# Optimization experiments

Hardware: AMD Instinct MI355X
Metric: run time of the kernel (lower is better)

Reference implementation:

```python
import jax, jax.numpy as jnp
import numpy as np

B, CIN, H, W = 32, 512, 64, 64
HID, A, C = 256, 9, 20
M = 65536


def setup_inputs() -> dict:
    key = jax.random.key(0)
    k = jax.random.split(key, 7)
    N = B * A * H * W
    features = jax.random.normal(k[0], (B, CIN, H, W), jnp.float32)
    W1 = jax.random.normal(k[1], (HID, CIN), jnp.float32) * 0.02
    b1 = jnp.zeros((HID,), jnp.float32)
    W2 = jax.random.normal(k[2], (5 * A + C, HID), jnp.float32) * 0.02
    b2 = jnp.zeros((5 * A + C,), jnp.float32)
    pos_anchor_idx = jax.random.randint(k[3], (M,), 0, N, jnp.int64 if jax.config.read('jax_enable_x64') else jnp.int32)
    neg_anchor_idx = jax.random.randint(k[4], (M,), 0, N, jnp.int64 if jax.config.read('jax_enable_x64') else jnp.int32)
    return {"features": features, "W1": W1, "b1": b1, "W2": W2, "b2": b2,
            "pos_anchor_idx": pos_anchor_idx, "neg_anchor_idx": neg_anchor_idx}


def reference(features, W1, b1, W2, b2, pos_anchor_idx, neg_anchor_idx):
    Bb, Cin, Hh, Ww = features.shape
    # 1x1 convs are channel GEMMs
    h = jnp.einsum('bchw,oc->bohw', features, W1) + b1[None, :, None, None]
    h = jax.nn.leaky_relu(h, 0.01)  # Dropout2d identity at inference
    out = jnp.einsum('bchw,oc->bohw', h, W2) + b2[None, :, None, None]
    class_scores = out[:, 5 * A:, :, :]                      # (B, C, H, W)
    anchor = out[:, :5 * A, :, :].reshape(Bb, A, 5, Hh, Ww)   # (B, A, 5, H, W)
    conf = jax.nn.sigmoid(anchor[:, :, 0:1])                  # (B, A, 1, H, W)
    off = anchor[:, :, 1:]                                    # (B, A, 4, H, W)
    off = jnp.concatenate([jax.nn.sigmoid(off[:, :, :2]) - 0.5, off[:, :, 2:]], axis=2)
    # extraction: flat layout is b*A*H*W + a*H*W + h*W + w (permute 0,1,3,4,2)
    off_flat = off.transpose(0, 1, 3, 4, 2).reshape(-1, 4)
    conf_flat = conf.transpose(0, 1, 3, 4, 2).reshape(-1, 1)
    offsets = off_flat[pos_anchor_idx]                        # (M, 4)
    conf_out = jnp.concatenate([conf_flat[pos_anchor_idx], conf_flat[neg_anchor_idx]], axis=0)  # (2M, 1)
    # class scores: expand over A is a pure broadcast, so index by (b, spatial) directly
    b_idx = pos_anchor_idx // (A * Hh * Ww)
    sp = pos_anchor_idx % (Hh * Ww)
    cls_flat = class_scores.transpose(0, 2, 3, 1).reshape(Bb * Hh * Ww, -1)
    class_out = cls_flat[b_idx * (Hh * Ww) + sp]              # (M, C)
    return conf_out, offsets, class_out
```

## Files before the change

### kernel.cpp

```cpp
#include <hip/hip_runtime.h>
#include <hip/hip_bf16.h>

typedef __attribute__((ext_vector_type(8)))  __bf16 bf16x8;
typedef __attribute__((ext_vector_type(4)))  __bf16 bf16x4;
typedef __attribute__((ext_vector_type(16))) float  f32x16;
typedef __attribute__((ext_vector_type(4)))  float  f32x4;

#define B_    32
#define CIN   512
#define HID   256
#define HW    4096
#define NA    9
#define NCH   65
#define NPADC 96
#define BN    128
#define M_    65536
#define NTOT  (B_*NA*HW)

#define BAR() do {                                          \
    asm volatile("s_waitcnt lgkmcnt(0)" ::: "memory");      \
    __builtin_amdgcn_s_barrier();                           \
    __builtin_amdgcn_sched_barrier(0);                      \
} while (0)


static __device__ __forceinline__ float sigf(float v) {
    return 1.f / (1.f + __expf(-v));
}

__global__ void prep_weights(const float* __restrict__ W1, const float* __restrict__ W2,
                             unsigned short* __restrict__ W1bt, unsigned short* __restrict__ W2p) {
    int i = blockIdx.x * 256 + threadIdx.x;
    if (i < 16*256*32) {
        int kt = i >> 13, o = (i >> 5) & 255, kk = i & 31;
        __bf16 h = (__bf16)W1[o*CIN + kt*32 + kk];
        W1bt[i] = __builtin_bit_cast(unsigned short, h);
    } else {
        int j = i - 16*256*32;
        if (j < NPADC*HID) {
            int o = j >> 8, c = j & 255;
            float v = (o < NCH) ? W2[o*HID + c] : 0.f;
            __bf16 h = (__bf16)v;
            W2p[j] = __builtin_bit_cast(unsigned short, h);
        }
    }
}

__launch_bounds__(256, 2)
__global__ void fused_mlp(const float* __restrict__ feat,
                          const float* __restrict__ b1,
                          const float* __restrict__ b2,
                          const unsigned short* __restrict__ W1bt,
                          const unsigned short* __restrict__ W2p,
                          float* __restrict__ conf_d,
                          unsigned short* __restrict__ off_w,
                          unsigned short* __restrict__ cls_w) {
    __shared__ __align__(16) unsigned char smem[65536];

    const int tid  = threadIdx.x;
    const int w    = tid >> 6;
    const int lane = tid & 63;
    const int lr   = lane & 31;
    const int lh   = lane >> 5;
    const int bidx = blockIdx.x >> 5;
    const int hw0  = (blockIdx.x & 31) * BN;

    const float* fb = feat + (size_t)bidx * CIN * HW + hw0;

    const int sB  = tid & 127;
    const int kgB = tid >> 7;

    f32x16 acc[2][4];
#pragma unroll
    for (int m = 0; m < 2; ++m)
#pragma unroll
        for (int n = 0; n < 4; ++n) acc[m][n] = (f32x16)0.f;

    float  pb[2][16];
    bf16x8 aw[2][4];

    auto issueB = [&](int kt, int s) {
#pragma unroll
        for (int q = 0; q < 2; ++q) {
            const float* src = fb + (size_t)(kt*32 + (kgB + 2*q)*8) * HW + sB;
#pragma unroll
            for (int j = 0; j < 8; ++j) pb[s][q*8 + j] = src[(size_t)j * HW];
        }
    };
    auto issueA = [&](int kt, int s) {
#pragma unroll
        for (int kk = 0; kk < 2; ++kk)
#pragma unroll
            for (int m = 0; m < 2; ++m)
                aw[s][kk*2 + m] = *(const bf16x8*)(W1bt + kt*8192 + (64*w + 32*m + lr)*32 + kk*16 + lh*8);
    };
    auto storeB = [&](int s) {
        unsigned short* Bst = (unsigned short*)(smem + s*10240);
#pragma unroll
        for (int q = 0; q < 2; ++q) {
            bf16x8 v8;
#pragma unroll
            for (int j = 0; j < 8; ++j) v8[j] = (__bf16)pb[s][q*8 + j];
            *(bf16x8*)(Bst + sB*40 + (kgB + 2*q)*8) = v8;
        }
    };

    issueA(0, 0); issueB(0, 0); issueB(1, 1);
    storeB(0);
    BAR();

#pragma unroll
    for (int kt = 0; kt < 16; ++kt) {
        const int cur = kt & 1, nxt = cur ^ 1;
        if (kt + 1 < 16) issueA(kt + 1, nxt);
        if (kt + 2 < 16) issueB(kt + 2, cur);
        const unsigned short* Bst = (const unsigned short*)(smem + cur*10240);
#pragma unroll
        for (int kk = 0; kk < 2; ++kk) {
            bf16x8 a0 = aw[cur][kk*2 + 0];
            bf16x8 a1 = aw[cur][kk*2 + 1];
#pragma unroll
            for (int n = 0; n < 4; ++n) {
                bf16x8 bv = *(const bf16x8*)(Bst + (32*n + lr)*40 + kk*16 + lh*8);
                acc[0][n] = __builtin_amdgcn_mfma_f32_32x32x16_bf16(a0, bv, acc[0][n], 0, 0, 0);
                acc[1][n] = __builtin_amdgcn_mfma_f32_32x32x16_bf16(a1, bv, acc[1][n], 0, 0, 0);
            }
        }
        if (kt + 1 < 16) storeB(nxt);
        BAR();
    }

#pragma unroll
    for (int m = 0; m < 2; ++m)
#pragma unroll
        for (int n = 0; n < 4; ++n) {
            int col = 32*n + lr;
            unsigned cswz = (unsigned)((col & 7) << 4);
#pragma unroll
            for (int g = 0; g < 4; ++g) {
                int rbase = 64*w + 32*m + 8*g + 4*lh;
                f32x4 b1v = *(const f32x4*)(b1 + rbase);
                bf16x4 pk;
#pragma unroll
                for (int r = 0; r < 4; ++r) {
                    float v = acc[m][n][4*g + r] + b1v[r];
                    v = v > 0.f ? v : 0.01f * v;
                    pk[r] = (__bf16)v;
                }
                unsigned addr = (unsigned)(col*512 + rbase*2) ^ cswz;
                *(bf16x4*)(smem + addr) = pk;
            }
        }
    BAR();

    f32x16 acc2[3];
#pragma unroll
    for (int m = 0; m < 3; ++m) acc2[m] = (f32x16)0.f;
    const int col2 = 32*w + lr;
    const unsigned cswz2 = (unsigned)((col2 & 7) << 4);
    for (int kt2 = 0; kt2 < 8; ++kt2) {
#pragma unroll
        for (int kk = 0; kk < 2; ++kk) {
            int k0 = kt2*32 + kk*16 + lh*8;
            bf16x8 bv = *(const bf16x8*)(smem + ((unsigned)(col2*512 + k0*2) ^ cswz2));
#pragma unroll
            for (int m = 0; m < 3; ++m) {
                bf16x8 av = *(const bf16x8*)(W2p + (32*m + lr)*256 + k0);
                acc2[m] = __builtin_amdgcn_mfma_f32_32x32x16_bf16(av, bv, acc2[m], 0, 0, 0);
            }
        }
    }

    BAR();
    float* so = (float*)smem;
#pragma unroll
    for (int m = 0; m < 3; ++m)
#pragma unroll
        for (int g = 0; g < 4; ++g) {
            int rbase = 32*m + 8*g + 4*lh;
            if (rbase <= 64) {
#pragma unroll
                for (int r = 0; r < 4; ++r) {
                    int row = rbase + r;
                    if (row < NCH) so[row*128 + col2] = acc2[m][4*g + r] + b2[row];
                }
            }
        }
    BAR();

    {
        const int p   = tid & 127;
        const int phw = hw0 + p;
        const int b9  = bidx * NA;
        if (tid < 128) {
#pragma unroll
            for (int a = 0; a < 9; ++a) {
                float v0 = so[(5*a+0)*128 + p];
                float v1 = so[(5*a+1)*128 + p];
                float v2 = so[(5*a+2)*128 + p];
                float v3 = so[(5*a+3)*128 + p];
                float v4 = so[(5*a+4)*128 + p];
                int abase = ((b9 + a) << 12) + phw;
                conf_d[abase] = sigf(v0);
                bf16x4 o;
                o[0] = (__bf16)(sigf(v1) - 0.5f);
                o[1] = (__bf16)(sigf(v2) - 0.5f);
                o[2] = (__bf16)v3;
                o[3] = (__bf16)v4;
                *(bf16x4*)(off_w + ((size_t)abase << 2)) = o;
            }
        } else {
            unsigned short* dst = cls_w + ((size_t)((bidx << 12) + phw) << 5);
#pragma unroll
            for (int q = 0; q < 4; ++q) {
                bf16x8 v;
#pragma unroll
                for (int r = 0; r < 8; ++r) {
                    int c = q*8 + r;
                    v[r] = (c < 20) ? (__bf16)so[(45 + c)*128 + p] : (__bf16)0.f;
                }
                *(bf16x8*)(dst + q*8) = v;
            }
        }
    }
}

__global__ void gather_all(const int* __restrict__ pos, const int* __restrict__ neg,
                           const float* __restrict__ conf_d,
                           const unsigned short* __restrict__ off_w,
                           const unsigned short* __restrict__ cls_w,
                           float* __restrict__ out) {
    int t = blockIdx.x * 256 + threadIdx.x;
    if (t < 2*M_) {
        int idx = (t < M_) ? pos[t] : neg[t - M_];
        out[t] = conf_d[idx];
    } else if (t < 3*M_) {
        int i = t - 2*M_;
        int p = pos[i];
        bf16x4 o = *(const bf16x4*)(off_w + ((size_t)p << 2));
        f32x4 f;
        f[0] = (float)o[0]; f[1] = (float)o[1];
        f[2] = (float)o[2]; f[3] = (float)o[3];
        *(f32x4*)(out + 2*(size_t)M_ + 4*(size_t)i) = f;
    } else {
        int i = t - 3*M_;
        int p = pos[i];
        int hw = p & 4095;
        int b  = (p >> 12) / 9;
        const unsigned short* src = cls_w + ((size_t)((b << 12) + hw) << 5);
        float* dst = out + 6*(size_t)M_ + 20*(size_t)i;
        bf16x8 v0 = *(const bf16x8*)(src);
        bf16x8 v1 = *(const bf16x8*)(src + 8);
        bf16x4 v2 = *(const bf16x4*)(src + 16);
        f32x4 f;
        f[0] = (float)v0[0]; f[1] = (float)v0[1]; f[2] = (float)v0[2]; f[3] = (float)v0[3];
        *(f32x4*)(dst) = f;
        f[0] = (float)v0[4]; f[1] = (float)v0[5]; f[2] = (float)v0[6]; f[3] = (float)v0[7];
        *(f32x4*)(dst + 4) = f;
        f[0] = (float)v1[0]; f[1] = (float)v1[1]; f[2] = (float)v1[2]; f[3] = (float)v1[3];
        *(f32x4*)(dst + 8) = f;
        f[0] = (float)v1[4]; f[1] = (float)v1[5]; f[2] = (float)v1[6]; f[3] = (float)v1[7];
        *(f32x4*)(dst + 12) = f;
        f[0] = (float)v2[0]; f[1] = (float)v2[1]; f[2] = (float)v2[2]; f[3] = (float)v2[3];
        *(f32x4*)(dst + 16) = f;
    }
}

extern "C" void kernel_launch(void* const* d_in, const int* in_sizes, int n_in,
                              void* d_out, int out_size, void* d_ws, size_t ws_size,
                              hipStream_t stream) {
    const float* feat = (const float*)d_in[0];
    const float* W1   = (const float*)d_in[1];
    const float* b1   = (const float*)d_in[2];
    const float* W2   = (const float*)d_in[3];
    const float* b2   = (const float*)d_in[4];
    const int*   pos  = (const int*)d_in[5];
    const int*   neg  = (const int*)d_in[6];
    float* out = (float*)d_out;

    char* ws = (char*)d_ws;
    unsigned short* W1bt = (unsigned short*)ws;
    unsigned short* W2p  = (unsigned short*)(ws + 262144);
    float*          conf_d = (float*)(ws + 311296);
    unsigned short* off_w  = (unsigned short*)(ws + 5029888);
    unsigned short* cls_w  = (unsigned short*)(ws + 14467072);

    prep_weights<<<608, 256, 0, stream>>>(W1, W2, W1bt, W2p);
    fused_mlp<<<1024, 256, 0, stream>>>(feat, b1, b2, W1bt, W2p, conf_d, off_w, cls_w);
    gather_all<<<1024, 256, 0, stream>>>(pos, neg, conf_d, off_w, cls_w, out);
}
```

Measured before the change: 92.18 us.

## Double block tile to 256 pixels with 512 threads and split second GEMM per half

The fused MLP kernel now uses 512-thread blocks, each covering 256 spatial positions, and arranges its 8 waves as 4 hidden-row groups by 2 pixel halves. Each W1 fragment loaded from global memory is reused across twice as many pixels, and the grid drops from 1024 to 512 blocks. The second GEMM and the epilogue run twice, once per 128-pixel half, with all 8 waves sharing each half (W2 padded to 128 rows). This adds extra barriers and serialises the two halves. Fewer, larger blocks also risk lower occupancy and worse tail balance on the CUs.

```diff
diff --git a/kernel.cpp b/kernel.cpp
--- a/kernel.cpp
+++ b/kernel.cpp
@@ -12,8 +12,8 @@
 #define HW    4096
 #define NA    9
 #define NCH   65
-#define NPADC 96
-#define BN    128
+#define NPADC 128
+#define BN    256
 #define M_    65536
 #define NTOT  (B_*NA*HW)
 
@@ -46,7 +46,7 @@
     }
 }
 
-__launch_bounds__(256, 2)
+__launch_bounds__(512, 2)
 __global__ void fused_mlp(const float* __restrict__ feat,
                           const float* __restrict__ b1,
                           const float* __restrict__ b2,
@@ -62,13 +62,15 @@
     const int lane = tid & 63;
     const int lr   = lane & 31;
     const int lh   = lane >> 5;
-    const int bidx = blockIdx.x >> 5;
-    const int hw0  = (blockIdx.x & 31) * BN;
+    const int mg   = w >> 1;
+    const int ng   = w & 1;
+    const int bidx = blockIdx.x >> 4;
+    const int hw0  = (blockIdx.x & 15) * BN;
 
     const float* fb = feat + (size_t)bidx * CIN * HW + hw0;
 
-    const int sB  = tid & 127;
-    const int kgB = tid >> 7;
+    const int sB  = tid & 255;
+    const int kgB = tid >> 8;
 
     f32x16 acc[2][4];
 #pragma unroll
@@ -92,10 +94,10 @@
         for (int kk = 0; kk < 2; ++kk)
 #pragma unroll
             for (int m = 0; m < 2; ++m)
-                aw[s][kk*2 + m] = *(const bf16x8*)(W1bt + kt*8192 + (64*w + 32*m + lr)*32 + kk*16 + lh*8);
+                aw[s][kk*2 + m] = *(const bf16x8*)(W1bt + kt*8192 + (64*mg + 32*m + lr)*32 + kk*16 + lh*8);
     };
     auto storeB = [&](int s) {
-        unsigned short* Bst = (unsigned short*)(smem + s*10240);
+        unsigned short* Bst = (unsigned short*)(smem + s*20480);
 #pragma unroll
         for (int q = 0; q < 2; ++q) {
             bf16x8 v8;
@@ -114,14 +116,14 @@
         const int cur = kt & 1, nxt = cur ^ 1;
         if (kt + 1 < 16) issueA(kt + 1, nxt);
         if (kt + 2 < 16) issueB(kt + 2, cur);
-        const unsigned short* Bst = (const unsigned short*)(smem + cur*10240);
+        const unsigned short* Bst = (const unsigned short*)(smem + cur*20480);
 #pragma unroll
         for (int kk = 0; kk < 2; ++kk) {
             bf16x8 a0 = aw[cur][kk*2 + 0];
             bf16x8 a1 = aw[cur][kk*2 + 1];
 #pragma unroll
             for (int n = 0; n < 4; ++n) {
-                bf16x8 bv = *(const bf16x8*)(Bst + (32*n + lr)*40 + kk*16 + lh*8);
+                bf16x8 bv = *(const bf16x8*)(Bst + (128*ng + 32*n + lr)*40 + kk*16 + lh*8);
                 acc[0][n] = __builtin_amdgcn_mfma_f32_32x32x16_bf16(a0, bv, acc[0][n], 0, 0, 0);
                 acc[1][n] = __builtin_amdgcn_mfma_f32_32x32x16_bf16(a1, bv, acc[1][n], 0, 0, 0);
             }
@@ -131,97 +133,104 @@
     }
 
 #pragma unroll
-    for (int m = 0; m < 2; ++m)
-#pragma unroll
-        for (int n = 0; n < 4; ++n) {
-            int col = 32*n + lr;
-            unsigned cswz = (unsigned)((col & 7) << 4);
+    for (int p = 0; p < 2; ++p) {
+        if (ng == p) {
+#pragma unroll
+            for (int m = 0; m < 2; ++m)
+#pragma unroll
+                for (int n = 0; n < 4; ++n) {
+                    int c = 32*n + lr;
+                    unsigned cswz = (unsigned)((c & 7) << 4);
+#pragma unroll
+                    for (int g = 0; g < 4; ++g) {
+                        int rbase = 64*mg + 32*m + 8*g + 4*lh;
+                        f32x4 b1v = *(const f32x4*)(b1 + rbase);
+                        bf16x4 pk;
+#pragma unroll
+                        for (int r = 0; r < 4; ++r) {
+                            float v = acc[m][n][4*g + r] + b1v[r];
+                            v = v > 0.f ? v : 0.01f * v;
+                            pk[r] = (__bf16)v;
+                        }
+                        *(bf16x4*)(smem + ((unsigned)(c*512 + rbase*2) ^ cswz)) = pk;
+                    }
+                }
+        }
+        BAR();
+
+        f32x16 acc2[2];
+#pragma unroll
+        for (int m = 0; m < 2; ++m) acc2[m] = (f32x16)0.f;
+        const int colh = w & 3, rowh = w >> 2;
+        const int col2 = 32*colh + lr;
+        const unsigned cswz2 = (unsigned)((col2 & 7) << 4);
+#pragma unroll
+        for (int kt2 = 0; kt2 < 8; ++kt2) {
+#pragma unroll
+            for (int kk = 0; kk < 2; ++kk) {
+                int k0 = kt2*32 + kk*16 + lh*8;
+                bf16x8 bv2 = *(const bf16x8*)(smem + ((unsigned)(col2*512 + k0*2) ^ cswz2));
+#pragma unroll
+                for (int m = 0; m < 2; ++m) {
+                    bf16x8 av = *(const bf16x8*)(W2p + (64*rowh + 32*m + lr)*256 + k0);
+                    acc2[m] = __builtin_amdgcn_mfma_f32_32x32x16_bf16(av, bv2, acc2[m], 0, 0, 0);
+                }
+            }
+        }
+        BAR();
+
+        float* so = (float*)smem;
+#pragma unroll
+        for (int m = 0; m < 2; ++m)
 #pragma unroll
             for (int g = 0; g < 4; ++g) {
-                int rbase = 64*w + 32*m + 8*g + 4*lh;
-                f32x4 b1v = *(const f32x4*)(b1 + rbase);
-                bf16x4 pk;
-#pragma unroll
-                for (int r = 0; r < 4; ++r) {
-                    float v = acc[m][n][4*g + r] + b1v[r];
-                    v = v > 0.f ? v : 0.01f * v;
-                    pk[r] = (__bf16)v;
-                }
-                unsigned addr = (unsigned)(col*512 + rbase*2) ^ cswz;
-                *(bf16x4*)(smem + addr) = pk;
+                int rbase = 64*rowh + 32*m + 8*g + 4*lh;
+                if (rbase <= 64) {
+#pragma unroll
+                    for (int r = 0; r < 4; ++r) {
+                        int row = rbase + r;
+                        if (row < NCH) so[row*128 + col2] = acc2[m][4*g + r] + b2[row];
+                    }
+                }
             }
-        }
-    BAR();
-
-    f32x16 acc2[3];
-#pragma unroll
-    for (int m = 0; m < 3; ++m) acc2[m] = (f32x16)0.f;
-    const int col2 = 32*w + lr;
-    const unsigned cswz2 = (unsigned)((col2 & 7) << 4);
-    for (int kt2 = 0; kt2 < 8; ++kt2) {
-#pragma unroll
-        for (int kk = 0; kk < 2; ++kk) {
-            int k0 = kt2*32 + kk*16 + lh*8;
-            bf16x8 bv = *(const bf16x8*)(smem + ((unsigned)(col2*512 + k0*2) ^ cswz2));
-#pragma unroll
-            for (int m = 0; m < 3; ++m) {
-                bf16x8 av = *(const bf16x8*)(W2p + (32*m + lr)*256 + k0);
-                acc2[m] = __builtin_amdgcn_mfma_f32_32x32x16_bf16(av, bv, acc2[m], 0, 0, 0);
+        BAR();
+
+        {
+            const int pp  = tid & 127;
+            const int phw = hw0 + 128*p + pp;
+            const int b9  = bidx * NA;
+            if (tid < 128) {
+#pragma unroll
+                for (int a = 0; a < 9; ++a) {
+                    float v0 = so[(5*a+0)*128 + pp];
+                    float v1 = so[(5*a+1)*128 + pp];
+                    float v2 = so[(5*a+2)*128 + pp];
+                    float v3 = so[(5*a+3)*128 + pp];
+                    float v4 = so[(5*a+4)*128 + pp];
+                    int abase = ((b9 + a) << 12) + phw;
+                    conf_d[abase] = sigf(v0);
+                    bf16x4 o;
+                    o[0] = (__bf16)(sigf(v1) - 0.5f);
+                    o[1] = (__bf16)(sigf(v2) - 0.5f);
+                    o[2] = (__bf16)v3;
+                    o[3] = (__bf16)v4;
+                    *(bf16x4*)(off_w + ((size_t)abase << 2)) = o;
+                }
+            } else if (tid < 256) {
+                unsigned short* dst = cls_w + ((size_t)((bidx << 12) + phw) << 5);
+#pragma unroll
+                for (int q = 0; q < 4; ++q) {
+                    bf16x8 v;
+#pragma unroll
+                    for (int r = 0; r < 8; ++r) {
+                        int c = q*8 + r;
+                        v[r] = (c < 20) ? (__bf16)so[(45 + c)*128 + pp] : (__bf16)0.f;
+                    }
+                    *(bf16x8*)(dst + q*8) = v;
+                }
             }
         }
-    }
-
-    BAR();
-    float* so = (float*)smem;
-#pragma unroll
-    for (int m = 0; m < 3; ++m)
-#pragma unroll
-        for (int g = 0; g < 4; ++g) {
-            int rbase = 32*m + 8*g + 4*lh;
-            if (rbase <= 64) {
-#pragma unroll
-                for (int r = 0; r < 4; ++r) {
-                    int row = rbase + r;
-                    if (row < NCH) so[row*128 + col2] = acc2[m][4*g + r] + b2[row];
-                }
-            }
-        }
-    BAR();
-
-    {
-        const int p   = tid & 127;
-        const int phw = hw0 + p;
-        const int b9  = bidx * NA;
-        if (tid < 128) {
-#pragma unroll
-            for (int a = 0; a < 9; ++a) {
-                float v0 = so[(5*a+0)*128 + p];
-                float v1 = so[(5*a+1)*128 + p];
-                float v2 = so[(5*a+2)*128 + p];
-                float v3 = so[(5*a+3)*128 + p];
-                float v4 = so[(5*a+4)*128 + p];
-                int abase = ((b9 + a) << 12) + phw;
-                conf_d[abase] = sigf(v0);
-                bf16x4 o;
-                o[0] = (__bf16)(sigf(v1) - 0.5f);
-                o[1] = (__bf16)(sigf(v2) - 0.5f);
-                o[2] = (__bf16)v3;
-                o[3] = (__bf16)v4;
-                *(bf16x4*)(off_w + ((size_t)abase << 2)) = o;
-            }
-        } else {
-            unsigned short* dst = cls_w + ((size_t)((bidx << 12) + phw) << 5);
-#pragma unroll
-            for (int q = 0; q < 4; ++q) {
-                bf16x8 v;
-#pragma unroll
-                for (int r = 0; r < 8; ++r) {
-                    int c = q*8 + r;
-                    v[r] = (c < 20) ? (__bf16)so[(45 + c)*128 + p] : (__bf16)0.f;
-                }
-                *(bf16x8*)(dst + q*8) = v;
-            }
-        }
+        BAR();
     }
 }
 
@@ -281,11 +290,11 @@
     char* ws = (char*)d_ws;
     unsigned short* W1bt = (unsigned short*)ws;
     unsigned short* W2p  = (unsigned short*)(ws + 262144);
-    float*          conf_d = (float*)(ws + 311296);
-    unsigned short* off_w  = (unsigned short*)(ws + 5029888);
-    unsigned short* cls_w  = (unsigned short*)(ws + 14467072);
-
-    prep_weights<<<608, 256, 0, stream>>>(W1, W2, W1bt, W2p);
-    fused_mlp<<<1024, 256, 0, stream>>>(feat, b1, b2, W1bt, W2p, conf_d, off_w, cls_w);
+    float*          conf_d = (float*)(ws + 327680);
+    unsigned short* off_w  = (unsigned short*)(ws + 5046272);
+    unsigned short* cls_w  = (unsigned short*)(ws + 14483456);
+
+    prep_weights<<<640, 256, 0, stream>>>(W1, W2, W1bt, W2p);
+    fused_mlp<<<512, 512, 0, stream>>>(feat, b1, b2, W1bt, W2p, conf_d, off_w, cls_w);
     gather_all<<<1024, 256, 0, stream>>>(pos, neg, conf_d, off_w, cls_w, out);
 }
```

After: 121.8 us. 1.32x slower.
